# Kernel optimization log

Hardware: AMD Instinct MI355X
Metric: run time of the kernel (lower is better)

## Reference

```python
import jax, jax.numpy as jnp
import numpy as np

INPUT_SIZE = 5
HIDDEN = 5
OUT = 1


def setup_inputs() -> dict:
    key = jax.random.key(0)
    ks = jax.random.split(key, 10)
    B, T = 8192, 512
    s_ih = 1.0 / np.sqrt(HIDDEN)
    inp = {
        "x": jax.random.normal(ks[0], (B, T, INPUT_SIZE), dtype=jnp.float32),
        # PyTorch LSTM params: gate order i, f, g, o
        "W_ih": jax.random.uniform(ks[1], (4 * HIDDEN, INPUT_SIZE), minval=-s_ih, maxval=s_ih, dtype=jnp.float32),
        "W_hh": jax.random.uniform(ks[2], (4 * HIDDEN, HIDDEN), minval=-s_ih, maxval=s_ih, dtype=jnp.float32),
        "b_ih": jax.random.uniform(ks[3], (4 * HIDDEN,), minval=-s_ih, maxval=s_ih, dtype=jnp.float32),
        "b_hh": jax.random.uniform(ks[4], (4 * HIDDEN,), minval=-s_ih, maxval=s_ih, dtype=jnp.float32),
        "fc1_w": jax.random.uniform(ks[5], (OUT, HIDDEN), minval=-s_ih, maxval=s_ih, dtype=jnp.float32),
        "fc1_b": jax.random.uniform(ks[6], (OUT,), minval=-s_ih, maxval=s_ih, dtype=jnp.float32),
        "fc2_w": jax.random.uniform(ks[7], (OUT, HIDDEN), minval=-s_ih, maxval=s_ih, dtype=jnp.float32),
        "fc2_b": jax.random.uniform(ks[8], (OUT,), minval=-s_ih, maxval=s_ih, dtype=jnp.float32),
    }
    return inp


def _lstm_last_hidden(x, W_ih, W_hh, b_ih, b_hh):
    # Precompute input contribution for all timesteps in one big GEMM:
    # [B, T, 4H]
    gates_x = jnp.einsum("bti,gi->btg", x, W_ih) + (b_ih + b_hh)
    B = x.shape[0]
    h0 = jnp.zeros((B, HIDDEN), dtype=x.dtype)
    c0 = jnp.zeros((B, HIDDEN), dtype=x.dtype)

    def step(carry, gx):
        h, c = carry
        g = gx + h @ W_hh.T  # [B, 4H]
        i = jax.nn.sigmoid(g[:, 0 * HIDDEN:1 * HIDDEN])
        f = jax.nn.sigmoid(g[:, 1 * HIDDEN:2 * HIDDEN])
        gg = jnp.tanh(g[:, 2 * HIDDEN:3 * HIDDEN])
        o = jax.nn.sigmoid(g[:, 3 * HIDDEN:4 * HIDDEN])
        c_new = f * c + i * gg
        h_new = o * jnp.tanh(c_new)
        return (h_new, c_new), None

    (h_last, _), _ = jax.lax.scan(step, (h0, c0), jnp.swapaxes(gates_x, 0, 1))
    return h_last  # [B, H]


def reference(x, W_ih, W_hh, b_ih, b_hh, fc1_w, fc1_b, fc2_w, fc2_b):
    h = _lstm_last_hidden(x, W_ih, W_hh, b_ih, b_hh)  # out[:, -1, :]
    price = h @ fc1_w.T + fc1_b
    volume = h @ fc2_w.T + fc2_b
    return (price, volume)
```

## Files before the change

kernel.cpp:

```cpp
#include <hip/hip_runtime.h>

#define BTOT 8192
#define TT 512
#define LOG2E 1.44269504089f

__device__ __forceinline__ float rcp_f(float x)  { return __builtin_amdgcn_rcpf(x); }
__device__ __forceinline__ float exp2_f(float x) { return __builtin_amdgcn_exp2f(x); }
__device__ __forceinline__ float bperm(int addr4, float v) {
    return __int_as_float(__builtin_amdgcn_ds_bpermute(addr4, __float_as_int(v)));
}
template<int CTRL>
__device__ __forceinline__ float qb(float v) {
    return __int_as_float(__builtin_amdgcn_mov_dpp(__float_as_int(v), CTRL, 0xf, 0xf, true));
}

__global__ __launch_bounds__(64) void lstm_kernel(
    const float* __restrict__ x,
    const float* __restrict__ W_ih,
    const float* __restrict__ W_hh,
    const float* __restrict__ b_ih,
    const float* __restrict__ b_hh,
    const float* __restrict__ fc1_w,
    const float* __restrict__ fc1_b,
    const float* __restrict__ fc2_w,
    const float* __restrict__ fc2_b,
    float* __restrict__ out)
{
    const int lane   = threadIdx.x;
    const int ll     = (lane < 60) ? lane : 59;
    const int bw     = ll / 20;
    const int within = ll % 20;
    const int j      = within >> 2;
    const int g      = within & 3;
    const int base   = bw * 20;
    const int b_raw  = blockIdx.x * 3 + bw;
    const bool write_ok = (lane < 60) && (within == 0) && (b_raw < BTOT);
    const int b = (b_raw < BTOT) ? b_raw : (BTOT - 1);

    const float sc   = (g == 2) ? (2.0f * LOG2E) : (-LOG2E);
    const float selA = (g == 2) ? -2.0f :  1.0f;
    const float selB = (g == 2) ?  1.0f :  0.0f;

    const int row = g * 5 + j;
    float wih[5], whh[5];
    #pragma unroll
    for (int i = 0; i < 5; ++i) {
        wih[i] = sc * W_ih[row * 5 + i];
        whh[i] = sc * W_hh[row * 5 + i];
    }
    const float bias_s = sc * (b_ih[row] + b_hh[row]);

    int a_h[5];
    #pragma unroll
    for (int k = 0; k < 5; ++k) a_h[k] = (base + 4 * k) << 2;

    const float* xb = x + (size_t)b * (TT * 5);

    float hv[5] = {0.f, 0.f, 0.f, 0.f, 0.f};
    float c = 0.f;

    float4 bufA[5], bufB[5];
    #pragma unroll
    for (int i = 0; i < 5; ++i) {
        bufA[i] = *(const float4*)(xb + 0  + 4 * i);
        bufB[i] = *(const float4*)(xb + 20 + 4 * i);
    }

    auto process4 = [&](const float4* buf) {
        float xs[20];
        *(float4*)&xs[0]  = buf[0];
        *(float4*)&xs[4]  = buf[1];
        *(float4*)&xs[8]  = buf[2];
        *(float4*)&xs[12] = buf[3];
        *(float4*)&xs[16] = buf[4];

        float gx[4];
        #pragma unroll
        for (int s = 0; s < 4; ++s) {
            float a = bias_s;
            #pragma unroll
            for (int i = 0; i < 5; ++i) a = fmaf(wih[i], xs[s * 5 + i], a);
            gx[s] = a;
        }

        #pragma unroll
        for (int s = 0; s < 4; ++s) {
            float acc = gx[s];
            #pragma unroll
            for (int k = 0; k < 5; ++k) acc = fmaf(whh[k], hv[k], acc);
            const float val = fmaf(selA, rcp_f(1.0f + exp2_f(acc)), selB);

            const float iv = qb<0x00>(val);
            const float fv = qb<0x55>(val);
            const float gv = qb<0xAA>(val);
            const float ov = qb<0xFF>(val);

            c = fmaf(fv, c, iv * gv);
            const float ec = exp2_f(c * (2.0f * LOG2E));
            const float tc = fmaf(-2.0f, rcp_f(1.0f + ec), 1.0f);
            const float h  = ov * tc;

            #pragma unroll
            for (int k = 0; k < 5; ++k) hv[k] = bperm(a_h[k], h);
        }
    };

    for (int t0 = 0; t0 < TT; t0 += 8) {
        process4(bufA);
        {
            const int tld = (t0 + 8 <= TT - 4) ? (t0 + 8) : (TT - 4);
            const float* p = xb + tld * 5;
            #pragma unroll
            for (int i = 0; i < 5; ++i) bufA[i] = *(const float4*)(p + 4 * i);
        }
        process4(bufB);
        {
            const int tld = (t0 + 12 <= TT - 4) ? (t0 + 12) : (TT - 4);
            const float* p = xb + tld * 5;
            #pragma unroll
            for (int i = 0; i < 5; ++i) bufB[i] = *(const float4*)(p + 4 * i);
        }
    }

    if (write_ok) {
        float p = fc1_b[0];
        float v = fc2_b[0];
        #pragma unroll
        for (int k = 0; k < 5; ++k) {
            p = fmaf(fc1_w[k], hv[k], p);
            v = fmaf(fc2_w[k], hv[k], v);
        }
        out[b] = p;
        out[BTOT + b] = v;
    }
}

extern "C" void kernel_launch(void* const* d_in, const int* in_sizes, int n_in,
                              void* d_out, int out_size, void* d_ws, size_t ws_size,
                              hipStream_t stream) {
    const float* x     = (const float*)d_in[0];
    const float* W_ih  = (const float*)d_in[1];
    const float* W_hh  = (const float*)d_in[2];
    const float* b_ih  = (const float*)d_in[3];
    const float* b_hh  = (const float*)d_in[4];
    const float* fc1_w = (const float*)d_in[5];
    const float* fc1_b = (const float*)d_in[6];
    const float* fc2_w = (const float*)d_in[7];
    const float* fc2_b = (const float*)d_in[8];
    float* out = (float*)d_out;

    const int blocks = (BTOT + 2) / 3;
    lstm_kernel<<<blocks, 64, 0, stream>>>(x, W_ih, W_hh, b_ih, b_hh,
                                           fc1_w, fc1_b, fc2_w, fc2_b, out);
}
```

Baseline: 114.3 us.

## Replace transcendental builtins with polynomial exp2/rcp and stagger block starts

```diff
diff --git a/kernel.cpp b/kernel.cpp
--- a/kernel.cpp
+++ b/kernel.cpp
@@ -4,14 +4,35 @@
 #define TT 512
 #define LOG2E 1.44269504089f
 
-__device__ __forceinline__ float rcp_f(float x)  { return __builtin_amdgcn_rcpf(x); }
-__device__ __forceinline__ float exp2_f(float x) { return __builtin_amdgcn_exp2f(x); }
 __device__ __forceinline__ float bperm(int addr4, float v) {
     return __int_as_float(__builtin_amdgcn_ds_bpermute(addr4, __float_as_int(v)));
 }
 template<int CTRL>
 __device__ __forceinline__ float qb(float v) {
     return __int_as_float(__builtin_amdgcn_mov_dpp(__float_as_int(v), CTRL, 0xf, 0xf, true));
+}
+
+__device__ __forceinline__ float soft_exp2(float t) {
+    t = __builtin_amdgcn_fmed3f(t, -30.0f, 30.0f);
+    const float n = floorf(t);
+    const float f = t - n;
+    float p = fmaf(f, 0.0013333558f, 0.0096181291f);
+    p = fmaf(p, f, 0.0555041087f);
+    p = fmaf(p, f, 0.2402265070f);
+    p = fmaf(p, f, 0.6931471806f);
+    p = fmaf(p, f, 1.0f);
+    return ldexpf(p, (int)n);
+}
+
+__device__ __forceinline__ float soft_rcp1p(float E) {
+    const float d = 1.0f + E;
+    const int bi = __float_as_int(d);
+    const int e  = (bi >> 23) - 127;
+    const float m = __int_as_float((bi & 0x007FFFFF) | 0x3F800000);
+    float r = fmaf(m, -0.47058824f, 1.41176471f);
+    r = r * fmaf(-m, r, 2.0f);
+    r = r * fmaf(-m, r, 2.0f);
+    return __int_as_float(__float_as_int(r) - (e << 23));
 }
 
 __global__ __launch_bounds__(64) void lstm_kernel(
@@ -26,6 +47,13 @@
     const float* __restrict__ fc2_b,
     float* __restrict__ out)
 {
+    switch (blockIdx.x & 3) {
+        case 1: __builtin_amdgcn_s_sleep(2); break;
+        case 2: __builtin_amdgcn_s_sleep(4); break;
+        case 3: __builtin_amdgcn_s_sleep(6); break;
+        default: break;
+    }
+
     const int lane   = threadIdx.x;
     const int ll     = (lane < 60) ? lane : 59;
     const int bw     = ll / 20;
@@ -38,8 +66,8 @@
     const int b = (b_raw < BTOT) ? b_raw : (BTOT - 1);
 
     const float sc   = (g == 2) ? (2.0f * LOG2E) : (-LOG2E);
-    const float selA = (g == 2) ? -2.0f :  1.0f;
-    const float selB = (g == 2) ?  1.0f :  0.0f;
+    const float selA = (g == 2) ? (-4.0f * LOG2E) : 1.0f;
+    const float selB = (g == 2) ? ( 2.0f * LOG2E) : 0.0f;
 
     const int row = g * 5 + j;
     float wih[5], whh[5];
@@ -57,7 +85,7 @@
     const float* xb = x + (size_t)b * (TT * 5);
 
     float hv[5] = {0.f, 0.f, 0.f, 0.f, 0.f};
-    float c = 0.f;
+    float C = 0.f;
 
     float4 bufA[5], bufB[5];
     #pragma unroll
@@ -74,34 +102,35 @@
         *(float4*)&xs[12] = buf[3];
         *(float4*)&xs[16] = buf[4];
 
-        float gx[4];
-        #pragma unroll
-        for (int s = 0; s < 4; ++s) {
+        auto proj = [&](int s) {
             float a = bias_s;
             #pragma unroll
             for (int i = 0; i < 5; ++i) a = fmaf(wih[i], xs[s * 5 + i], a);
-            gx[s] = a;
-        }
+            return a;
+        };
 
+        float gxc = proj(0);
         #pragma unroll
         for (int s = 0; s < 4; ++s) {
-            float acc = gx[s];
+            float acc = gxc;
             #pragma unroll
             for (int k = 0; k < 5; ++k) acc = fmaf(whh[k], hv[k], acc);
-            const float val = fmaf(selA, rcp_f(1.0f + exp2_f(acc)), selB);
+            const float r1  = soft_rcp1p(soft_exp2(acc));
+            const float val = fmaf(selA, r1, selB);
 
             const float iv = qb<0x00>(val);
             const float fv = qb<0x55>(val);
             const float gv = qb<0xAA>(val);
             const float ov = qb<0xFF>(val);
 
-            c = fmaf(fv, c, iv * gv);
-            const float ec = exp2_f(c * (2.0f * LOG2E));
-            const float tc = fmaf(-2.0f, rcp_f(1.0f + ec), 1.0f);
-            const float h  = ov * tc;
+            C = fmaf(fv, C, iv * gv);
+            const float r2 = soft_rcp1p(soft_exp2(C));
+            const float h  = ov * fmaf(-2.0f, r2, 1.0f);
 
             #pragma unroll
             for (int k = 0; k < 5; ++k) hv[k] = bperm(a_h[k], h);
+
+            if (s < 3) gxc = proj(s + 1);
         }
     };
 
```

New measurement: 153.6 us. 34.3% more time.

## Interleave two independent batch sequences per lane group to hide recurrence latency

Applied to the files above, without the earlier changes.

```diff
diff --git a/kernel.cpp b/kernel.cpp
--- a/kernel.cpp
+++ b/kernel.cpp
@@ -33,9 +33,11 @@
     const int j      = within >> 2;
     const int g      = within & 3;
     const int base   = bw * 20;
-    const int b_raw  = blockIdx.x * 3 + bw;
-    const bool write_ok = (lane < 60) && (within == 0) && (b_raw < BTOT);
-    const int b = (b_raw < BTOT) ? b_raw : (BTOT - 1);
+
+    const int bA_raw = blockIdx.x * 6 + bw * 2;
+    const int bB_raw = bA_raw + 1;
+    const int bA = (bA_raw < BTOT) ? bA_raw : (BTOT - 1);
+    const int bB = (bB_raw < BTOT) ? bB_raw : (BTOT - 1);
 
     const float sc   = (g == 2) ? (2.0f * LOG2E) : (-LOG2E);
     const float selA = (g == 2) ? -2.0f :  1.0f;
@@ -54,84 +56,112 @@
     #pragma unroll
     for (int k = 0; k < 5; ++k) a_h[k] = (base + 4 * k) << 2;
 
-    const float* xb = x + (size_t)b * (TT * 5);
+    const float* xA = x + (size_t)bA * (TT * 5);
+    const float* xB = x + (size_t)bB * (TT * 5);
 
-    float hv[5] = {0.f, 0.f, 0.f, 0.f, 0.f};
-    float c = 0.f;
+    float hvA[5] = {0.f, 0.f, 0.f, 0.f, 0.f};
+    float hvB[5] = {0.f, 0.f, 0.f, 0.f, 0.f};
+    float CA = 0.f, CB = 0.f;
 
     float4 bufA[5], bufB[5];
     #pragma unroll
     for (int i = 0; i < 5; ++i) {
-        bufA[i] = *(const float4*)(xb + 0  + 4 * i);
-        bufB[i] = *(const float4*)(xb + 20 + 4 * i);
+        bufA[i] = *(const float4*)(xA + 4 * i);
+        bufB[i] = *(const float4*)(xB + 4 * i);
     }
 
-    auto process4 = [&](const float4* buf) {
-        float xs[20];
-        *(float4*)&xs[0]  = buf[0];
-        *(float4*)&xs[4]  = buf[1];
-        *(float4*)&xs[8]  = buf[2];
-        *(float4*)&xs[12] = buf[3];
-        *(float4*)&xs[16] = buf[4];
+    auto bufAt = [](const float4* buf, int idx) -> float {
+        const float4 v = buf[idx >> 2];
+        switch (idx & 3) {
+            case 0: return v.x;
+            case 1: return v.y;
+            case 2: return v.z;
+            default: return v.w;
+        }
+    };
 
-        float gx[4];
+    for (int t0 = 0; t0 < TT; t0 += 4) {
+        float gxA[4], gxB[4];
         #pragma unroll
         for (int s = 0; s < 4; ++s) {
-            float a = bias_s;
+            float aA = bias_s, aB = bias_s;
             #pragma unroll
-            for (int i = 0; i < 5; ++i) a = fmaf(wih[i], xs[s * 5 + i], a);
-            gx[s] = a;
+            for (int i = 0; i < 5; ++i) {
+                aA = fmaf(wih[i], bufAt(bufA, s * 5 + i), aA);
+                aB = fmaf(wih[i], bufAt(bufB, s * 5 + i), aB);
+            }
+            gxA[s] = aA; gxB[s] = aB;
+        }
+
+        {
+            const int tld = (t0 + 4 <= TT - 4) ? (t0 + 4) : (TT - 4);
+            const float* pA = xA + tld * 5;
+            const float* pB = xB + tld * 5;
+            #pragma unroll
+            for (int i = 0; i < 5; ++i) {
+                bufA[i] = *(const float4*)(pA + 4 * i);
+                bufB[i] = *(const float4*)(pB + 4 * i);
+            }
         }
 
         #pragma unroll
         for (int s = 0; s < 4; ++s) {
-            float acc = gx[s];
-            #pragma unroll
-            for (int k = 0; k < 5; ++k) acc = fmaf(whh[k], hv[k], acc);
-            const float val = fmaf(selA, rcp_f(1.0f + exp2_f(acc)), selB);
-
-            const float iv = qb<0x00>(val);
-            const float fv = qb<0x55>(val);
-            const float gv = qb<0xAA>(val);
-            const float ov = qb<0xFF>(val);
-
-            c = fmaf(fv, c, iv * gv);
-            const float ec = exp2_f(c * (2.0f * LOG2E));
-            const float tc = fmaf(-2.0f, rcp_f(1.0f + ec), 1.0f);
-            const float h  = ov * tc;
-
-            #pragma unroll
-            for (int k = 0; k < 5; ++k) hv[k] = bperm(a_h[k], h);
-        }
-    };
-
-    for (int t0 = 0; t0 < TT; t0 += 8) {
-        process4(bufA);
-        {
-            const int tld = (t0 + 8 <= TT - 4) ? (t0 + 8) : (TT - 4);
-            const float* p = xb + tld * 5;
-            #pragma unroll
-            for (int i = 0; i < 5; ++i) bufA[i] = *(const float4*)(p + 4 * i);
-        }
-        process4(bufB);
-        {
-            const int tld = (t0 + 12 <= TT - 4) ? (t0 + 12) : (TT - 4);
-            const float* p = xb + tld * 5;
-            #pragma unroll
-            for (int i = 0; i < 5; ++i) bufB[i] = *(const float4*)(p + 4 * i);
+            {
+                float acc = gxA[s];
+                #pragma unroll
+                for (int k = 0; k < 5; ++k) acc = fmaf(whh[k], hvA[k], acc);
+                const float val = fmaf(selA, rcp_f(1.0f + exp2_f(acc)), selB);
+                const float iv = qb<0x00>(val);
+                const float fv = qb<0x55>(val);
+                const float gv = qb<0xAA>(val);
+                const float ov = qb<0xFF>(val);
+                CA = fmaf(fv, CA, iv * gv);
+                const float ec = exp2_f(CA * (2.0f * LOG2E));
+                const float h  = ov * fmaf(-2.0f, rcp_f(1.0f + ec), 1.0f);
+                #pragma unroll
+                for (int k = 0; k < 5; ++k) hvA[k] = bperm(a_h[k], h);
+            }
+            {
+                float acc = gxB[s];
+                #pragma unroll
+                for (int k = 0; k < 5; ++k) acc = fmaf(whh[k], hvB[k], acc);
+                const float val = fmaf(selA, rcp_f(1.0f + exp2_f(acc)), selB);
+                const float iv = qb<0x00>(val);
+                const float fv = qb<0x55>(val);
+                const float gv = qb<0xAA>(val);
+                const float ov = qb<0xFF>(val);
+                CB = fmaf(fv, CB, iv * gv);
+                const float ec = exp2_f(CB * (2.0f * LOG2E));
+                const float h  = ov * fmaf(-2.0f, rcp_f(1.0f + ec), 1.0f);
+                #pragma unroll
+                for (int k = 0; k < 5; ++k) hvB[k] = bperm(a_h[k], h);
+            }
         }
     }
 
-    if (write_ok) {
-        float p = fc1_b[0];
-        float v = fc2_b[0];
-        #pragma unroll
-        for (int k = 0; k < 5; ++k) {
-            p = fmaf(fc1_w[k], hv[k], p);
-            v = fmaf(fc2_w[k], hv[k], v);
+    if (lane < 60) {
+        if (within == 0 && bA_raw < BTOT) {
+            float p = fc1_b[0];
+            float v = fc2_b[0];
+            #pragma unroll
+            for (int k = 0; k < 5; ++k) {
+                p = fmaf(fc1_w[k], hvA[k], p);
+                v = fmaf(fc2_w[k], hvA[k], v);
+            }
+            out[bA] = p;
+            out[BTOT + bA] = v;
         }
-        out[b] = p;
-        out[BTOT + b] = v;
+        if (within == 1 && bB_raw < BTOT) {
+            float p = fc1_b[0];
+            float v = fc2_b[0];
+            #pragma unroll
+            for (int k = 0; k < 5; ++k) {
+                p = fmaf(fc1_w[k], hvB[k], p);
+                v = fmaf(fc2_w[k], hvB[k], v);
+            }
+            out[bB] = p;
+            out[BTOT + bB] = v;
+        }
     }
 }
 
@@ -149,7 +179,7 @@
     const float* fc2_b = (const float*)d_in[8];
     float* out = (float*)d_out;
 
-    const int blocks = (BTOT + 2) / 3;
+    const int blocks = (BTOT + 5) / 6;
     lstm_kernel<<<blocks, 64, 0, stream>>>(x, W_ih, W_hh, b_ih, b_hh,
                                            fc1_w, fc1_b, fc2_w, fc2_b, out);
 }
```

Result: slower. 191.7 us (+67.7%).
